# Kernel optimization log

Measured on AMD Instinct MI355X. Metric: run time of the kernel, lower is better.

Reference implementation:

```python
import math
import jax, jax.numpy as jnp
import numpy as np

SEQ_LEN = 512
K_MAX = 32


def setup_inputs() -> dict:
    key = jax.random.key(0)
    spectral = jax.random.normal(key, (4, 512, 64, K_MAX, 2), dtype=jnp.float32)
    return {"spectral": spectral}


def reference(spectral) -> jnp.ndarray:
    # spectral: (batch, T, d_spectral, k_max, 2)
    B, T, D, K, _ = spectral.shape
    dt = spectral.dtype
    # normalization == 'position': scale by sqrt(t+1) per source position t
    pos_inv_norm = jnp.sqrt(jnp.arange(1, T + 1, dtype=dt))  # (T,)
    s = spectral * pos_inv_norm[None, :, None, None, None]
    # inverse twiddles: angles[n, k] = 2*pi*n*k / seq_len
    n = jnp.arange(SEQ_LEN, dtype=dt)
    k = jnp.arange(K, dtype=dt)
    angles = (2.0 * math.pi / SEQ_LEN) * jnp.outer(n, k)  # (seq_len, k_max)
    t_real = jnp.cos(angles)
    t_imag = jnp.sin(angles)
    # real part of complex contraction over k, as a GEMM instead of the
    # huge broadcast intermediate the torch code materializes
    out_real = (
        jnp.einsum("btdk,nk->btnd", s[..., 0], t_real)
        - jnp.einsum("btdk,nk->btnd", s[..., 1], t_imag)
    ) / SEQ_LEN
    return out_real  # (batch, T, seq_len, d_spectral)
```

## Files before the change

### kernel.cpp

```cpp
#include <hip/hip_runtime.h>
#include <stdint.h>


typedef short bf16x8 __attribute__((ext_vector_type(8)));
typedef float f32x4  __attribute__((ext_vector_type(4)));

__device__ __forceinline__ unsigned short f2bf(float f) {
    union { float f; uint32_t u; } v; v.f = f;
    uint32_t u = v.u;
    u += 0x7fffu + ((u >> 16) & 1u);
    return (unsigned short)(u >> 16);
}

__global__ void build_twiddle(unsigned short* __restrict__ T) {
    int gid = blockIdx.x * blockDim.x + threadIdx.x;
    int n   = gid >> 6;
    int kk  = gid & 63;
    int k   = kk >> 1;
    int m   = (n * k) & 511;
    float ang = (float)m * (6.283185307179586f / 512.0f);
    float val = (kk & 1) ? __sinf(ang) : __cosf(ang);
    val = (kk & 1) ? sinf(ang) : cosf(ang);
    T[gid] = f2bf(val);
}

__global__ __launch_bounds__(256) void cum_ifft(
    const float* __restrict__ spectral,
    const unsigned short* __restrict__ T,
    float* __restrict__ out)
{
    __shared__ unsigned short S[64 * 72];
    const int bt  = blockIdx.x;
    const int tid = threadIdx.x;
    const int t   = bt & 511;
    const float scale = sqrtf((float)(t + 1)) * (1.0f / 512.0f);

    const float4* src = (const float4*)(spectral + (size_t)bt * 4096);
    #pragma unroll
    for (int it = 0; it < 4; ++it) {
        int idx = it * 256 + tid;
        int d   = idx >> 4;
        int k2  = idx & 15;
        float4 v = src[idx];
        unsigned int w0 = (unsigned int)f2bf(v.x * scale) |
                          ((unsigned int)f2bf(-v.y * scale) << 16);
        unsigned int w1 = (unsigned int)f2bf(v.z * scale) |
                          ((unsigned int)f2bf(-v.w * scale) << 16);
        unsigned int* dst = (unsigned int*)(&S[d * 72 + k2 * 4]);
        dst[0] = w0; dst[1] = w1;
    }
    __syncthreads();

    const int lane = tid & 63;
    const int w    = tid >> 6;
    const int lrow = lane & 15;
    const int quad = lane >> 4;

    bf16x8 bfrag[4][2];
    #pragma unroll
    for (int dt = 0; dt < 4; ++dt)
        #pragma unroll
        for (int ks = 0; ks < 2; ++ks)
            bfrag[dt][ks] = *(const bf16x8*)(&S[(dt * 16 + lrow) * 72 + ks * 32 + quad * 8]);

    bf16x8 afrag[8][2];
    #pragma unroll
    for (int i = 0; i < 8; ++i) {
        int n = (w * 8 + i) * 16 + lrow;
        #pragma unroll
        for (int ks = 0; ks < 2; ++ks)
            afrag[i][ks] = *(const bf16x8*)(&T[n * 64 + ks * 32 + quad * 8]);
    }

    float* outp = out + (size_t)bt * (512 * 64);
    #pragma unroll
    for (int i = 0; i < 8; ++i) {
        int n0 = (w * 8 + i) * 16;
        #pragma unroll
        for (int dt = 0; dt < 4; ++dt) {
            f32x4 acc = {0.f, 0.f, 0.f, 0.f};
            acc = __builtin_amdgcn_mfma_f32_16x16x32_bf16(afrag[i][0], bfrag[dt][0], acc, 0, 0, 0);
            acc = __builtin_amdgcn_mfma_f32_16x16x32_bf16(afrag[i][1], bfrag[dt][1], acc, 0, 0, 0);
            int col   = dt * 16 + lrow;
            int rbase = n0 + quad * 4;
            #pragma unroll
            for (int r = 0; r < 4; ++r)
                outp[(size_t)(rbase + r) * 64 + col] = acc[r];
        }
    }
}

extern "C" void kernel_launch(void* const* d_in, const int* in_sizes, int n_in,
                              void* d_out, int out_size, void* d_ws, size_t ws_size,
                              hipStream_t stream) {
    const float* spectral = (const float*)d_in[0];
    unsigned short* T     = (unsigned short*)d_ws;
    float* out            = (float*)d_out;

    build_twiddle<<<128, 256, 0, stream>>>(T);
    cum_ifft<<<2048, 256, 0, stream>>>(spectral, T, out);
}
```

Measured before the change: 303.9 us.

## Stage MFMA outputs through LDS for 16-byte nontemporal stores, prefetch twiddles

Each wave now writes its 16x64 MFMA accumulator tile to a padded per-wave LDS buffer, then reads it back as float4 rows and issues 16-byte nontemporal global stores. Previously it issued scattered 4-byte stores. The twiddle fragments are software-pipelined, loading one row-tile ahead instead of all eight up front, and launch bounds request 4 blocks per CU. The goal is better store coalescing and less cache pollution on the large write-only output, at the cost of extra LDS traffic and waitcnt serialisation.

```diff
diff --git a/kernel.cpp b/kernel.cpp
--- a/kernel.cpp
+++ b/kernel.cpp
@@ -19,17 +19,17 @@
     int k   = kk >> 1;
     int m   = (n * k) & 511;
     float ang = (float)m * (6.283185307179586f / 512.0f);
-    float val = (kk & 1) ? __sinf(ang) : __cosf(ang);
-    val = (kk & 1) ? sinf(ang) : cosf(ang);
+    float val = (kk & 1) ? sinf(ang) : cosf(ang);
     T[gid] = f2bf(val);
 }
 
-__global__ __launch_bounds__(256) void cum_ifft(
+__global__ __launch_bounds__(256, 4) void cum_ifft(
     const float* __restrict__ spectral,
     const unsigned short* __restrict__ T,
     float* __restrict__ out)
 {
     __shared__ unsigned short S[64 * 72];
+    __shared__ float XP[4][16 * 68];
     const int bt  = blockIdx.x;
     const int tid = threadIdx.x;
     const int t   = bt & 511;
@@ -46,8 +46,8 @@
                           ((unsigned int)f2bf(-v.y * scale) << 16);
         unsigned int w1 = (unsigned int)f2bf(v.z * scale) |
                           ((unsigned int)f2bf(-v.w * scale) << 16);
-        unsigned int* dst = (unsigned int*)(&S[d * 72 + k2 * 4]);
-        dst[0] = w0; dst[1] = w1;
+        uint2* dst = (uint2*)(&S[d * 72 + k2 * 4]);
+        *dst = make_uint2(w0, w1);
     }
     __syncthreads();
 
@@ -63,30 +63,54 @@
         for (int ks = 0; ks < 2; ++ks)
             bfrag[dt][ks] = *(const bf16x8*)(&S[(dt * 16 + lrow) * 72 + ks * 32 + quad * 8]);
 
-    bf16x8 afrag[8][2];
-    #pragma unroll
+    float* outp = out + (size_t)bt * (512 * 64);
+    float* xp   = &XP[w][0];
+
+    int n0 = (w * 8) * 16;
+    bf16x8 a0 = *(const bf16x8*)(&T[(n0 + lrow) * 64 + quad * 8]);
+    bf16x8 a1 = *(const bf16x8*)(&T[(n0 + lrow) * 64 + 32 + quad * 8]);
+
     for (int i = 0; i < 8; ++i) {
-        int n = (w * 8 + i) * 16 + lrow;
+        bf16x8 na0, na1;
+        if (i < 7) {
+            int nn = (w * 8 + i + 1) * 16 + lrow;
+            na0 = *(const bf16x8*)(&T[nn * 64 + quad * 8]);
+            na1 = *(const bf16x8*)(&T[nn * 64 + 32 + quad * 8]);
+        }
+
+        f32x4 acc0 = {0.f, 0.f, 0.f, 0.f};
+        f32x4 acc1 = {0.f, 0.f, 0.f, 0.f};
+        f32x4 acc2 = {0.f, 0.f, 0.f, 0.f};
+        f32x4 acc3 = {0.f, 0.f, 0.f, 0.f};
+        acc0 = __builtin_amdgcn_mfma_f32_16x16x32_bf16(a0, bfrag[0][0], acc0, 0, 0, 0);
+        acc1 = __builtin_amdgcn_mfma_f32_16x16x32_bf16(a0, bfrag[1][0], acc1, 0, 0, 0);
+        acc2 = __builtin_amdgcn_mfma_f32_16x16x32_bf16(a0, bfrag[2][0], acc2, 0, 0, 0);
+        acc3 = __builtin_amdgcn_mfma_f32_16x16x32_bf16(a0, bfrag[3][0], acc3, 0, 0, 0);
+        acc0 = __builtin_amdgcn_mfma_f32_16x16x32_bf16(a1, bfrag[0][1], acc0, 0, 0, 0);
+        acc1 = __builtin_amdgcn_mfma_f32_16x16x32_bf16(a1, bfrag[1][1], acc1, 0, 0, 0);
+        acc2 = __builtin_amdgcn_mfma_f32_16x16x32_bf16(a1, bfrag[2][1], acc2, 0, 0, 0);
+        acc3 = __builtin_amdgcn_mfma_f32_16x16x32_bf16(a1, bfrag[3][1], acc3, 0, 0, 0);
+
         #pragma unroll
-        for (int ks = 0; ks < 2; ++ks)
-            afrag[i][ks] = *(const bf16x8*)(&T[n * 64 + ks * 32 + quad * 8]);
-    }
+        for (int r = 0; r < 4; ++r) {
+            xp[(quad * 4 + r) * 68 +  0 + lrow] = acc0[r];
+            xp[(quad * 4 + r) * 68 + 16 + lrow] = acc1[r];
+            xp[(quad * 4 + r) * 68 + 32 + lrow] = acc2[r];
+            xp[(quad * 4 + r) * 68 + 48 + lrow] = acc3[r];
+        }
+        asm volatile("s_waitcnt lgkmcnt(0)" ::: "memory");
 
-    float* outp = out + (size_t)bt * (512 * 64);
-    #pragma unroll
-    for (int i = 0; i < 8; ++i) {
-        int n0 = (w * 8 + i) * 16;
+        int nrow = (w * 8 + i) * 16;
         #pragma unroll
-        for (int dt = 0; dt < 4; ++dt) {
-            f32x4 acc = {0.f, 0.f, 0.f, 0.f};
-            acc = __builtin_amdgcn_mfma_f32_16x16x32_bf16(afrag[i][0], bfrag[dt][0], acc, 0, 0, 0);
-            acc = __builtin_amdgcn_mfma_f32_16x16x32_bf16(afrag[i][1], bfrag[dt][1], acc, 0, 0, 0);
-            int col   = dt * 16 + lrow;
-            int rbase = n0 + quad * 4;
-            #pragma unroll
-            for (int r = 0; r < 4; ++r)
-                outp[(size_t)(rbase + r) * 64 + col] = acc[r];
+        for (int j = 0; j < 4; ++j) {
+            int row = j * 4 + quad;
+            f32x4 v = *(const f32x4*)(&xp[row * 68 + lrow * 4]);
+            __builtin_nontemporal_store(
+                v, (f32x4*)(outp + (size_t)(nrow + row) * 64 + lrow * 4));
         }
+        asm volatile("" ::: "memory");
+
+        a0 = na0; a1 = na1;
     }
 }
 
```

Result: faster. 285.0 us (-6.2%).
